# Kernel tuning notes

Measured on AMD Instinct MI355X. Metric: run time of the kernel, lower is better.

Reference implementation:

```python
import jax, jax.numpy as jnp
import numpy as np

EMBED_DIM = 1024
HEAD_SIZE = 64
B, T = 4, 4096


def setup_inputs() -> dict:
    key = jax.random.key(0)
    kx, kq, kk, kv = jax.random.split(key, 4)
    x = jax.random.normal(kx, (B, T, EMBED_DIM), dtype=jnp.float32)
    sw = 1.0 / np.sqrt(EMBED_DIM)  # kaiming-ish init scale for linear weights
    Wq = jax.random.normal(kq, (EMBED_DIM, HEAD_SIZE), dtype=jnp.float32) * sw
    Wk = jax.random.normal(kk, (EMBED_DIM, HEAD_SIZE), dtype=jnp.float32) * sw
    Wv = jax.random.normal(kv, (EMBED_DIM, HEAD_SIZE), dtype=jnp.float32) * sw
    return {"x": x, "Wq": Wq, "Wk": Wk, "Wv": Wv}


def reference(x, Wq, Wk, Wv):
    Bn, Tn, C = x.shape
    q = jnp.einsum('btc,ch->bth', x, Wq)
    k = jnp.einsum('btc,ch->bth', x, Wk)
    v = jnp.einsum('btc,ch->bth', x, Wv)
    # NOTE: original scales by sqrt(C) = sqrt(embed_dim), not sqrt(head_size)
    scale = 1.0 / jnp.sqrt(jnp.asarray(C, dtype=x.dtype))
    wei = jnp.einsum('bth,bsh->bts', q, k) * scale  # [B, T, T]
    causal = jnp.tril(jnp.ones((Tn, Tn), dtype=bool))
    wei = jnp.where(causal, wei, -jnp.inf)
    wei = jax.nn.softmax(wei, axis=-1)
    # dropout p=0.0 (eval mode): identity
    return jnp.einsum('bts,bsh->bth', wei, v)
```

## Files before the change

kernel.cpp:

```cpp
#include <hip/hip_runtime.h>
#include <cstdint>


typedef __bf16 bf16;
typedef __bf16 bf16x4 __attribute__((ext_vector_type(4)));
typedef __bf16 bf16x8 __attribute__((ext_vector_type(8)));
typedef float  f32x4  __attribute__((ext_vector_type(4)));

#define MFMA16(a, b, c) __builtin_amdgcn_mfma_f32_16x16x32_bf16((a), (b), (c), 0, 0, 0)

#if __has_builtin(__builtin_amdgcn_exp2f)
#define EXP2(x) __builtin_amdgcn_exp2f(x)
#else
#define EXP2(x) exp2f(x)
#endif

#define B_SZ 4
#define T_SZ 4096
#define C_SZ 1024
#define H_SZ 64
#define M_SZ (B_SZ * T_SZ)
#define QSCALE (1.4426950408889634f / 32.0f)
#define P_O 8192
#define P_L 128

__device__ __forceinline__ void dma16(const void* g, void* l) {
    __builtin_amdgcn_global_load_lds(
        (const __attribute__((address_space(1))) uint32_t*)(uintptr_t)g,
        (__attribute__((address_space(3))) uint32_t*)(uint32_t)(uintptr_t)l,
        16, 0, 0);
}

__device__ __forceinline__ void pipe_sync() {
    asm volatile("s_waitcnt vmcnt(0)" ::: "memory");
    __builtin_amdgcn_s_barrier();
    __builtin_amdgcn_sched_barrier(0);
}

__global__ __launch_bounds__(256) void wt_prep(
    const float* __restrict__ Wq, const float* __restrict__ Wk,
    const float* __restrict__ Wv, bf16* __restrict__ wt2)
{
    const int n4 = blockIdx.x, t = threadIdx.x;
    const int nbase = n4 * 4;
    const float* W = (nbase < 64) ? Wq : (nbase < 128 ? Wk : Wv);
    const float sc = (nbase < 64) ? QSCALE : 1.0f;
    const int ncol = nbase & 63;
    #pragma unroll
    for (int i = 0; i < 4; ++i) {
        const int k = i * 256 + t;
        const float4 v = *(const float4*)(W + (size_t)k * H_SZ + ncol);
        const float vals[4] = {v.x, v.y, v.z, v.w};
        const size_t base = (size_t)(k >> 6) * 12288 + (size_t)((k >> 5) & 1) * 6144
                          + (size_t)((k >> 3) & 3) * 1536 + (k & 7);
        #pragma unroll
        for (int m = 0; m < 4; ++m)
            wt2[base + (size_t)(nbase + m) * 8] = (bf16)(vals[m] * sc);
    }
}

__global__ __launch_bounds__(256) void qkv_proj(
    const float* __restrict__ x, const bf16* __restrict__ wt2,
    bf16* __restrict__ qw, bf16* __restrict__ kw2, bf16* __restrict__ vtw2)
{
    const int m0 = blockIdx.x * 32;
    const int tid = threadIdx.x;
    const int wave = tid >> 6, lane = tid & 63;
    const int quad = lane >> 4, l15 = lane & 15;
    const int phase = blockIdx.x & 15;

    __shared__ __align__(16) float xs[2 * 4 * 32 * 8];
    __shared__ __align__(16) bf16  ws[2 * 4 * 192 * 8];

    f32x4 acc[2][3] = {};

    const char* xg = (const char*)x
        + (size_t)(m0 + ((tid >> 1) & 31)) * 4096
        + (size_t)((tid >> 6) & 3) * 32 + (size_t)(tid & 1) * 16;
    char* xl = (char*)xs + (size_t)tid * 16;
    const char* wg = (const char*)wt2 + (size_t)tid * 16;
    char* wl = (char*)ws + (size_t)tid * 16;

    for (int s = 0; s < 16; ++s) {
        const size_t se = (size_t)((s + phase) & 15);
        __syncthreads();
        dma16(xg + se * 256, xl);
        dma16(xg + se * 256 + 128, xl + 4096);
        #pragma unroll
        for (int i = 0; i < 6; ++i)
            dma16(wg + se * 24576 + (size_t)i * 4096, wl + (size_t)i * 4096);
        __syncthreads();

        #pragma unroll
        for (int ss = 0; ss < 2; ++ss) {
            bf16x8 a[2];
            #pragma unroll
            for (int mg = 0; mg < 2; ++mg) {
                const float* ap = xs + ss * 1024 + quad * 256 + (mg * 16 + l15) * 8;
                const f32x4 lo = *(const f32x4*)ap;
                const f32x4 hi = *(const f32x4*)(ap + 4);
                a[mg][0] = (bf16)lo[0]; a[mg][1] = (bf16)lo[1];
                a[mg][2] = (bf16)lo[2]; a[mg][3] = (bf16)lo[3];
                a[mg][4] = (bf16)hi[0]; a[mg][5] = (bf16)hi[1];
                a[mg][6] = (bf16)hi[2]; a[mg][7] = (bf16)hi[3];
            }
            #pragma unroll
            for (int i = 0; i < 3; ++i) {
                const int nt = wave * 3 + i;
                const bf16x8 wf = *(const bf16x8*)(ws + ss * 6144 + quad * 1536
                                                   + (nt * 16 + l15) * 8);
                #pragma unroll
                for (int mg = 0; mg < 2; ++mg)
                    acc[mg][i] = MFMA16(a[mg], wf, acc[mg][i]);
            }
        }
    }

    #pragma unroll
    for (int mg = 0; mg < 2; ++mg)
        #pragma unroll
        for (int i = 0; i < 3; ++i) {
            const int n = (wave * 3 + i) * 16 + l15;
            const int which = n >> 6, col = n & 63;
            #pragma unroll
            for (int r = 0; r < 4; ++r) {
                const int t = m0 + mg * 16 + quad * 4 + r;
                const bf16 v = (bf16)acc[mg][i][r];
                if (which == 0) {
                    qw[(size_t)t * H_SZ + col] = v;
                } else if (which == 1) {
                    kw2[(size_t)(t >> 6) * 4096
                        + (size_t)(((col >> 5) << 2) + ((col >> 3) & 3)) * 512
                        + (size_t)(t & 63) * 8 + (col & 7)] = v;
                } else {
                    const int t6 = t & 63;
                    const int p = ((t6 & 15) << 2) | (t6 >> 4);
                    vtw2[(size_t)(t >> 6) * 4096
                         + (size_t)(p >> 3) * 512 + (size_t)col * 8 + (p & 7)] = v;
                }
            }
        }
}

__global__ __launch_bounds__(256) void flash_attn(
    const bf16* __restrict__ qw, const bf16* __restrict__ kw2,
    const bf16* __restrict__ vtw2, bf16* __restrict__ pbuf_o,
    float* __restrict__ pbuf_l)
{
    const int bx = blockIdx.x;
    const int item = (bx & 1) ? (511 - (bx >> 1)) : (bx >> 1);
    const int qt2 = 31 - (item >> 4);
    const int b   = (item >> 2) & 3;
    const int h   = item & 3;
    const int i0  = qt2 * 128;
    const int nkv = qt2 * 2 + 2;

    const int tid = threadIdx.x;
    const int wave = tid >> 6, lane = tid & 63;
    const int quad = lane >> 4, l15 = lane & 15;

    __shared__ __align__(16) bf16 kvs[2][8192];
    __shared__ __align__(16) bf16 pls[4][32 * 72];

    bf16x8 aq[2][2];
    #pragma unroll
    for (int mg2 = 0; mg2 < 2; ++mg2) {
        const bf16* qp = qw + ((size_t)b * T_SZ + i0 + wave * 32 + mg2 * 16 + l15) * H_SZ
                       + quad * 8;
        aq[mg2][0] = *(const bf16x8*)qp;
        aq[mg2][1] = *(const bf16x8*)(qp + 32);
    }
    const bf16 onev = (bf16)1.0f;
    const bf16x8 vone = {onev, onev, onev, onev, onev, onev, onev, onev};

    const char* kgb = (const char*)kw2 + (size_t)b * 524288;
    const char* vgb = (const char*)vtw2 + (size_t)b * 524288;
    bf16* pl = pls[wave];

    f32x4 o[2][4] = {};
    f32x4 osum[2] = {};

    auto stage = [&](int jt, int buf) {
        const char* ks = kgb + (size_t)jt * 8192;
        const char* vs = vgb + (size_t)jt * 8192;
        char* dst = (char*)(&kvs[buf][0]) + (size_t)tid * 16;
        dma16(ks + (size_t)tid * 16, dst);
        dma16(ks + 4096 + (size_t)tid * 16, dst + 4096);
        dma16(vs + (size_t)tid * 16, dst + 8192);
        dma16(vs + 4096 + (size_t)tid * 16, dst + 12288);
    };

    if (h < nkv) {
        stage(h, 0);
        pipe_sync();
    }

    int c = 0;
    for (int jt = h; jt < nkv; jt += 4, c ^= 1) {
        if (jt + 4 < nkv) stage(jt + 4, c ^ 1);
        const bf16* kb = &kvs[c][0];
        const bf16* vb = &kvs[c][0] + 4096;

        f32x4 s4[2][4] = {};
        __builtin_amdgcn_s_setprio(1);
        #pragma unroll
        for (int ct = 0; ct < 4; ++ct) {
            const bf16x8 k0 = *(const bf16x8*)(kb + (0 * 4 + quad) * 512 + (ct * 16 + l15) * 8);
            const bf16x8 k1 = *(const bf16x8*)(kb + (1 * 4 + quad) * 512 + (ct * 16 + l15) * 8);
            #pragma unroll
            for (int mg2 = 0; mg2 < 2; ++mg2) {
                s4[mg2][ct] = MFMA16(aq[mg2][0], k0, s4[mg2][ct]);
                s4[mg2][ct] = MFMA16(aq[mg2][1], k1, s4[mg2][ct]);
            }
        }
        __builtin_amdgcn_s_setprio(0);

        if (jt >= 2 * qt2) {
            #pragma unroll
            for (int mg2 = 0; mg2 < 2; ++mg2) {
                const int grow = i0 + wave * 32 + mg2 * 16 + quad * 4;
                #pragma unroll
                for (int ct = 0; ct < 4; ++ct) {
                    const int gcol = jt * 64 + ct * 16 + l15;
                    #pragma unroll
                    for (int rr = 0; rr < 4; ++rr)
                        if (gcol > grow + rr) s4[mg2][ct][rr] = -3.0e38f;
                }
            }
        }

        #pragma unroll
        for (int mg2 = 0; mg2 < 2; ++mg2)
            #pragma unroll
            for (int rr = 0; rr < 4; ++rr) {
                bf16x4 pk;
                pk[0] = (bf16)EXP2(s4[mg2][0][rr]);
                pk[1] = (bf16)EXP2(s4[mg2][1][rr]);
                pk[2] = (bf16)EXP2(s4[mg2][2][rr]);
                pk[3] = (bf16)EXP2(s4[mg2][3][rr]);
                *(bf16x4*)&pl[(mg2 * 16 + quad * 4 + rr) * 72 + l15 * 4] = pk;
            }

        bf16x8 pa[2][2];
        #pragma unroll
        for (int mg2 = 0; mg2 < 2; ++mg2) {
            pa[mg2][0] = *(const bf16x8*)&pl[(mg2 * 16 + l15) * 72 + quad * 8];
            pa[mg2][1] = *(const bf16x8*)&pl[(mg2 * 16 + l15) * 72 + 32 + quad * 8];
        }

        __builtin_amdgcn_s_setprio(1);
        #pragma unroll
        for (int ht = 0; ht < 4; ++ht) {
            const bf16x8 v0 = *(const bf16x8*)(vb + (0 * 4 + quad) * 512 + (ht * 16 + l15) * 8);
            const bf16x8 v1 = *(const bf16x8*)(vb + (1 * 4 + quad) * 512 + (ht * 16 + l15) * 8);
            #pragma unroll
            for (int mg2 = 0; mg2 < 2; ++mg2) {
                o[mg2][ht] = MFMA16(pa[mg2][0], v0, o[mg2][ht]);
                o[mg2][ht] = MFMA16(pa[mg2][1], v1, o[mg2][ht]);
            }
        }
        #pragma unroll
        for (int mg2 = 0; mg2 < 2; ++mg2) {
            osum[mg2] = MFMA16(pa[mg2][0], vone, osum[mg2]);
            osum[mg2] = MFMA16(pa[mg2][1], vone, osum[mg2]);
        }
        __builtin_amdgcn_s_setprio(0);

        pipe_sync();
    }

    bf16* pb_o = pbuf_o + (size_t)(((b * 32 + qt2) * 4) + h) * P_O;
    float* pb_l = pbuf_l + (size_t)(((b * 32 + qt2) * 4) + h) * P_L;
    #pragma unroll
    for (int mg2 = 0; mg2 < 2; ++mg2) {
        const int L0 = wave * 32 + mg2 * 16 + quad * 4;
        #pragma unroll
        for (int ht = 0; ht < 4; ++ht)
            #pragma unroll
            for (int rr = 0; rr < 4; ++rr)
                pb_o[(L0 + rr) * 64 + ht * 16 + l15] = (bf16)o[mg2][ht][rr];
        if (l15 == 0) {
            #pragma unroll
            for (int rr = 0; rr < 4; ++rr)
                pb_l[L0 + rr] = osum[mg2][rr];
        }
    }
}

__global__ __launch_bounds__(256) void combine(
    const bf16* __restrict__ pbuf_o, const float* __restrict__ pbuf_l,
    float* __restrict__ out)
{
    const int bq2 = blockIdx.x >> 1, tid = threadIdx.x;
    const int row = ((blockIdx.x & 1) << 6) + (tid >> 2);
    const int c0 = (tid & 3) * 16;

    float a[16] = {};
    float l = 0.f;
    #pragma unroll
    for (int h = 0; h < 4; ++h) {
        const bf16* ph = pbuf_o + (size_t)(bq2 * 4 + h) * P_O + row * 64 + c0;
        const bf16x8 v0 = *(const bf16x8*)ph;
        const bf16x8 v1 = *(const bf16x8*)(ph + 8);
        #pragma unroll
        for (int j = 0; j < 8; ++j) {
            a[j]     += (float)v0[j];
            a[8 + j] += (float)v1[j];
        }
        l += pbuf_l[(size_t)(bq2 * 4 + h) * P_L + row];
    }
    const float inv = 1.0f / l;
    float* op = out + ((size_t)bq2 * 128 + row) * 64 + c0;
    #pragma unroll
    for (int g = 0; g < 4; ++g) {
        f32x4 v = {a[g * 4], a[g * 4 + 1], a[g * 4 + 2], a[g * 4 + 3]};
        *(f32x4*)(op + g * 4) = v * inv;
    }
}

extern "C" void kernel_launch(void* const* d_in, const int* in_sizes, int n_in,
                              void* d_out, int out_size, void* d_ws, size_t ws_size,
                              hipStream_t stream) {
    const float* x  = (const float*)d_in[0];
    const float* Wq = (const float*)d_in[1];
    const float* Wk = (const float*)d_in[2];
    const float* Wv = (const float*)d_in[3];

    bf16* qw   = (bf16*)d_ws;
    bf16* kw2  = qw + (size_t)M_SZ * H_SZ;
    bf16* vtw2 = kw2 + (size_t)M_SZ * H_SZ;
    bf16* wt2  = vtw2 + (size_t)M_SZ * H_SZ;
    bf16* pbuf_o = wt2 + 3 * 64 * 1024;
    float* pbuf_l = (float*)(pbuf_o + (size_t)512 * P_O);
    float* out = (float*)d_out;

    wt_prep<<<48, 256, 0, stream>>>(Wq, Wk, Wv, wt2);
    qkv_proj<<<M_SZ / 32, 256, 0, stream>>>(x, wt2, qw, kw2, vtw2);
    flash_attn<<<512, 256, 0, stream>>>(qw, kw2, vtw2, pbuf_o, pbuf_l);
    combine<<<256, 256, 0, stream>>>(pbuf_o, pbuf_l, out);
}
```

Measured before the change: 143.8 us.

## Compute transposed S so P feeds PV MFMA from registers, drop LDS round-trip

Swaps the MFMA operands in the QK^T product so each lane holds S^T fragments whose elements line up with the A-operand layout needed for the P·V MFMA. The per-wave LDS buffer for P, with its writes and reads, is removed, and P is packed directly in registers. To make this work, the V^T layout written by the projection kernel is permuted to match the new key ordering inside each fragment. This cuts LDS traffic and shared memory per block, which may allow higher occupancy, but correctness depends on the permutation matching the fragment mapping exactly.

```diff
diff --git a/kernel.cpp b/kernel.cpp
--- a/kernel.cpp
+++ b/kernel.cpp
@@ -134,7 +134,8 @@
                         + (size_t)(t & 63) * 8 + (col & 7)] = v;
                 } else {
                     const int t6 = t & 63;
-                    const int p = ((t6 & 15) << 2) | (t6 >> 4);
+                    const int p = ((t6 >> 2) & 3) * 8 + (t6 & 3) * 2
+                                + ((t6 >> 4) & 1) + (t6 >> 5) * 32;
                     vtw2[(size_t)(t >> 6) * 4096
                          + (size_t)(p >> 3) * 512 + (size_t)col * 8 + (p & 7)] = v;
                 }
@@ -160,7 +161,6 @@
     const int quad = lane >> 4, l15 = lane & 15;
 
     __shared__ __align__(16) bf16 kvs[2][8192];
-    __shared__ __align__(16) bf16 pls[4][32 * 72];
 
     bf16x8 aq[2][2];
     #pragma unroll
@@ -175,7 +175,6 @@
 
     const char* kgb = (const char*)kw2 + (size_t)b * 524288;
     const char* vgb = (const char*)vtw2 + (size_t)b * 524288;
-    bf16* pl = pls[wave];
 
     f32x4 o[2][4] = {};
     f32x4 osum[2] = {};
@@ -201,7 +200,7 @@
         const bf16* kb = &kvs[c][0];
         const bf16* vb = &kvs[c][0] + 4096;
 
-        f32x4 s4[2][4] = {};
+        f32x4 s4t[4][2] = {};
         __builtin_amdgcn_s_setprio(1);
         #pragma unroll
         for (int ct = 0; ct < 4; ++ct) {
@@ -209,8 +208,8 @@
             const bf16x8 k1 = *(const bf16x8*)(kb + (1 * 4 + quad) * 512 + (ct * 16 + l15) * 8);
             #pragma unroll
             for (int mg2 = 0; mg2 < 2; ++mg2) {
-                s4[mg2][ct] = MFMA16(aq[mg2][0], k0, s4[mg2][ct]);
-                s4[mg2][ct] = MFMA16(aq[mg2][1], k1, s4[mg2][ct]);
+                s4t[ct][mg2] = MFMA16(k0, aq[mg2][0], s4t[ct][mg2]);
+                s4t[ct][mg2] = MFMA16(k1, aq[mg2][1], s4t[ct][mg2]);
             }
         }
         __builtin_amdgcn_s_setprio(0);
@@ -218,35 +217,25 @@
         if (jt >= 2 * qt2) {
             #pragma unroll
             for (int mg2 = 0; mg2 < 2; ++mg2) {
-                const int grow = i0 + wave * 32 + mg2 * 16 + quad * 4;
+                const int gq = i0 + wave * 32 + mg2 * 16 + l15;
                 #pragma unroll
                 for (int ct = 0; ct < 4; ++ct) {
-                    const int gcol = jt * 64 + ct * 16 + l15;
+                    const int gkv0 = jt * 64 + ct * 16 + quad * 4;
                     #pragma unroll
                     for (int rr = 0; rr < 4; ++rr)
-                        if (gcol > grow + rr) s4[mg2][ct][rr] = -3.0e38f;
+                        if (gkv0 + rr > gq) s4t[ct][mg2][rr] = -3.0e38f;
                 }
             }
         }
 
+        bf16x8 pa[2][2];
         #pragma unroll
         for (int mg2 = 0; mg2 < 2; ++mg2)
             #pragma unroll
-            for (int rr = 0; rr < 4; ++rr) {
-                bf16x4 pk;
-                pk[0] = (bf16)EXP2(s4[mg2][0][rr]);
-                pk[1] = (bf16)EXP2(s4[mg2][1][rr]);
-                pk[2] = (bf16)EXP2(s4[mg2][2][rr]);
-                pk[3] = (bf16)EXP2(s4[mg2][3][rr]);
-                *(bf16x4*)&pl[(mg2 * 16 + quad * 4 + rr) * 72 + l15 * 4] = pk;
-            }
-
-        bf16x8 pa[2][2];
-        #pragma unroll
-        for (int mg2 = 0; mg2 < 2; ++mg2) {
-            pa[mg2][0] = *(const bf16x8*)&pl[(mg2 * 16 + l15) * 72 + quad * 8];
-            pa[mg2][1] = *(const bf16x8*)&pl[(mg2 * 16 + l15) * 72 + 32 + quad * 8];
-        }
+            for (int j = 0; j < 8; ++j) {
+                pa[mg2][0][j] = (bf16)EXP2(s4t[j & 1][mg2][j >> 1]);
+                pa[mg2][1][j] = (bf16)EXP2(s4t[2 + (j & 1)][mg2][j >> 1]);
+            }
 
         __builtin_amdgcn_s_setprio(1);
         #pragma unroll
```

Measured after the change: 142.6 us. About the same (-0.8%).
